# Optimization experiments

Measured on AMD Instinct MI355X. Metric: run time of the kernel, lower is better.

Reference implementation:

```python
import jax, jax.numpy as jnp
import numpy as np
from jax import lax

NEG = -10000.0


def setup_inputs() -> dict:
    key = jax.random.key(0)
    ks = jax.random.split(key, 16)
    T, V, E, H, NT = 2048, 50000, 512, 512, 48  # H = per-direction hidden (hidden_dim//2)
    start, end = NT - 2, NT - 1

    def rn(k, shape, scale=0.05):
        return jax.random.normal(k, shape, jnp.float32) * scale

    words = jax.random.randint(ks[0], (T,), 0, V)
    embed = rn(ks[1], (V, E), 0.1)
    Wih_f = rn(ks[2], (4 * H, E)); Whh_f = rn(ks[3], (4 * H, H))
    bih_f = rn(ks[4], (4 * H,));   bhh_f = rn(ks[5], (4 * H,))
    Wih_b = rn(ks[6], (4 * H, E)); Whh_b = rn(ks[7], (4 * H, H))
    bih_b = rn(ks[8], (4 * H,));   bhh_b = rn(ks[9], (4 * H,))
    W_out = rn(ks[10], (NT, 2 * H)); b_out = rn(ks[11], (NT,))
    transitions = jax.random.normal(ks[12], (NT, NT), jnp.float32)
    # match __init__: no transition into START, none out of END
    transitions = transitions.at[start, :].set(NEG).at[:, end].set(NEG)
    h0 = rn(ks[13], (2, H), 1.0)  # [fwd, bwd] initial hidden (torch.randn in init_hidden)
    c0 = rn(ks[14], (2, H), 1.0)
    return dict(words=words, embed=embed,
                Wih_f=Wih_f, Whh_f=Whh_f, bih_f=bih_f, bhh_f=bhh_f,
                Wih_b=Wih_b, Whh_b=Whh_b, bih_b=bih_b, bhh_b=bhh_b,
                W_out=W_out, b_out=b_out, transitions=transitions,
                h0=h0, c0=c0, start_tag=start, end_tag=end)


def _lstm_dir(x, h0, c0, Wih, Whh, bih, bhh, reverse):
    # x: [T, E]. Precompute input contribution for all steps (one big GEMM).
    xW = x @ Wih.T + (bih + bhh)  # [T, 4H]

    def step(carry, g_in):
        h, c = carry
        g = g_in + h @ Whh.T  # [4H]
        i, f, gg, o = jnp.split(g, 4)
        i = jax.nn.sigmoid(i); f = jax.nn.sigmoid(f)
        gg = jnp.tanh(gg);     o = jax.nn.sigmoid(o)
        c = f * c + i * gg
        h = o * jnp.tanh(c)
        return (h, c), h

    _, hs = lax.scan(step, (h0, c0), xW, reverse=reverse)
    return hs  # [T, H], aligned with input time order


def reference(words, embed, Wih_f, Whh_f, bih_f, bhh_f,
              Wih_b, Whh_b, bih_b, bhh_b,
              W_out, b_out, transitions, h0, c0, start_tag, end_tag):
    x = embed[words]  # [T, E]
    hf = _lstm_dir(x, h0[0], c0[0], Wih_f, Whh_f, bih_f, bhh_f, reverse=False)
    hb = _lstm_dir(x, h0[1], c0[1], Wih_b, Whh_b, bih_b, bhh_b, reverse=True)
    frames = jnp.concatenate([hf, hb], axis=-1) @ W_out.T + b_out  # [T, NT] emissions

    nt = transitions.shape[0]
    tT = transitions.T  # tT[from, to]
    alpha0 = jnp.full((nt,), NEG, frames.dtype).at[start_tag].set(0.0)

    def vstep(alpha, frame):
        # smat[i, j] = alpha[i] + frame[j] + transitions[j, i]
        smat = alpha[:, None] + frame[None, :] + tT
        return smat.max(axis=0), jnp.argmax(smat, axis=0)

    alpha, backtrace = lax.scan(vstep, alpha0, frames)  # backtrace: [T, NT]
    final = alpha + transitions[end_tag]
    best_last = jnp.argmax(final)
    score = final[best_last]

    def back(tag, bp):
        prev = bp[tag]
        return prev, prev

    _, path_head = lax.scan(back, best_last, backtrace[1:], reverse=True)  # [T-1]
    best_path = jnp.concatenate([path_head, best_last[None]])  # [T]
    return score, best_path
```

## Files before the change

### kernel.cpp

```cpp
#include <hip/hip_runtime.h>

#define TT 2048
#define HH 512
#define EE 512
#define NTAGS 48
#define G4 2048
#define NWG 16
#define CANARY 1.0e30f

typedef float f4 __attribute__((ext_vector_type(4)));

#define OFF_XW    0ULL
#define OFF_HCAT  (OFF_XW   + 2ULL*TT*G4*4ULL)
#define OFF_FRM   (OFF_HCAT + (unsigned long long)TT*1024ULL*4ULL)
#define OFF_HBUF  (OFF_FRM  + (unsigned long long)TT*NTAGS*4ULL)
#define OFF_BP    (OFF_HBUF + 2ULL*4ULL*HH*4ULL)

__device__ __forceinline__ float fsig(float x) {
    return __builtin_amdgcn_rcpf(1.f + __expf(-x));
}
__device__ __forceinline__ float ftanh(float x) {
    return 1.f - 2.f*__builtin_amdgcn_rcpf(__expf(2.f*x) + 1.f);
}

__global__ __launch_bounds__(256) void k_xw(
    const int* __restrict__ words, const float* __restrict__ embed,
    const float* __restrict__ WihF, const float* __restrict__ WihB,
    const float* __restrict__ bihF, const float* __restrict__ bhhF,
    const float* __restrict__ bihB, const float* __restrict__ bhhB,
    float* __restrict__ xw, float* __restrict__ hbuf)
{
    const int tid = threadIdx.x;
    const int bx = blockIdx.x, by = blockIdx.y, dir = blockIdx.z;

    if (bx == 0 && by == 0) {
        for (int j = tid; j < 4*HH; j += 256)
            hbuf[dir*4*HH + j] = CANARY;
    }

    const float* Wih = dir ? WihB : WihF;
    const float* bi  = dir ? bihB : bihF;
    const float* bh  = dir ? bhhB : bhhF;

    __shared__ float sa[32][64];
    __shared__ float sb[32][64];
    __shared__ int   wds[64];
    if (tid < 64) wds[tid] = words[by*64 + tid];
    const int tx = tid & 15, ty = tid >> 4;
    float acc[4][4] = {};
    __syncthreads();

    for (int k0 = 0; k0 < EE; k0 += 32) {
        #pragma unroll
        for (int u = 0; u < 2; u++) {
            int idx = tid*2 + u;
            int row = idx >> 3, kq = idx & 7;
            float4 av = *(const float4*)&embed[(size_t)wds[row]*EE + k0 + kq*4];
            float4 bv = *(const float4*)&Wih[(size_t)(bx*64 + row)*EE + k0 + kq*4];
            sa[kq*4+0][row] = av.x; sa[kq*4+1][row] = av.y;
            sa[kq*4+2][row] = av.z; sa[kq*4+3][row] = av.w;
            sb[kq*4+0][row] = bv.x; sb[kq*4+1][row] = bv.y;
            sb[kq*4+2][row] = bv.z; sb[kq*4+3][row] = bv.w;
        }
        __syncthreads();
        #pragma unroll
        for (int k = 0; k < 32; k++) {
            float4 a = *(const float4*)&sa[k][ty*4];
            float4 b = *(const float4*)&sb[k][tx*4];
            acc[0][0] += a.x*b.x; acc[0][1] += a.x*b.y; acc[0][2] += a.x*b.z; acc[0][3] += a.x*b.w;
            acc[1][0] += a.y*b.x; acc[1][1] += a.y*b.y; acc[1][2] += a.y*b.z; acc[1][3] += a.y*b.w;
            acc[2][0] += a.z*b.x; acc[2][1] += a.z*b.y; acc[2][2] += a.z*b.z; acc[2][3] += a.z*b.w;
            acc[3][0] += a.w*b.x; acc[3][1] += a.w*b.y; acc[3][2] += a.w*b.z; acc[3][3] += a.w*b.w;
        }
        __syncthreads();
    }

    float* outp = xw + (size_t)dir*TT*G4;
    const int rbase = bx*64 + tx*4;
    float4 bi4 = *(const float4*)&bi[rbase];
    float4 bh4 = *(const float4*)&bh[rbase];
    float4 bias = make_float4(bi4.x+bh4.x, bi4.y+bh4.y, bi4.z+bh4.z, bi4.w+bh4.w);
    #pragma unroll
    for (int i = 0; i < 4; i++) {
        int t = by*64 + ty*4 + i;
        float4 v = make_float4(acc[i][0]+bias.x, acc[i][1]+bias.y,
                               acc[i][2]+bias.z, acc[i][3]+bias.w);
        *(float4*)&outp[(size_t)t*G4 + rbase] = v;
    }
}

__global__ __launch_bounds__(512, 2) void k_lstm(
    const float* __restrict__ WhhF, const float* __restrict__ WhhB,
    const float* __restrict__ h0, const float* __restrict__ c0,
    const float* __restrict__ xw,
    float* __restrict__ hbuf, float* __restrict__ hcat)
{
    const int bid = blockIdx.x;
    const int dir = bid >> 4;
    const int w   = bid & 15;
    const float* Whh = dir ? WhhB : WhhF;
    const float* xwD = xw + (size_t)dir*TT*G4;
    float* hb = hbuf + dir*4*HH;

    const int tid  = threadIdx.x;
    const int v    = tid >> 6;
    const int l    = tid & 63;
    const int hi   = l >> 4;
    const int k16  = l & 15;
    const int loc  = v*4 + hi;
    const int hidx = w*32 + loc;

    f4 wreg[4][8];
    {
        #pragma unroll
        for (int g = 0; g < 4; g++) {
            const f4* wr = (const f4*)&Whh[(size_t)(g*HH + hidx)*HH + k16*32];
            #pragma unroll
            for (int t = 0; t < 8; t++)
                asm volatile("global_load_dwordx4 %0, %1, off"
                             : "=v"(wreg[g][t]) : "v"(wr + t));
        }
        asm volatile("s_waitcnt vmcnt(0)" ::: "memory");
        __builtin_amdgcn_sched_barrier(0);
    }
    float c = 0.f;
    if (tid < 32) c = c0[dir*HH + w*32 + tid];

    __shared__ __align__(16) float hsh[2][16*36];
    __shared__ float gv[128];

    hsh[0][(tid>>5)*36 + (tid&31)] = h0[dir*HH + tid];
    __syncthreads();

    float xv = 0.f;
    if (k16 < 4) xv = xwD[(size_t)(dir ? TT-1 : 0)*G4 + k16*HH + hidx];

    for (int s = 0; s < TT; s++) {
        const float* hc = &hsh[s & 1][k16*36];
        f4 p = {0.f, 0.f, 0.f, 0.f};
        #pragma unroll
        for (int t = 0; t < 8; t++) {
            float4 hv = *(const float4*)&hc[4*t];
            p.x += wreg[0][t].x*hv.x; p.x += wreg[0][t].y*hv.y;
            p.x += wreg[0][t].z*hv.z; p.x += wreg[0][t].w*hv.w;
            p.y += wreg[1][t].x*hv.x; p.y += wreg[1][t].y*hv.y;
            p.y += wreg[1][t].z*hv.z; p.y += wreg[1][t].w*hv.w;
            p.z += wreg[2][t].x*hv.x; p.z += wreg[2][t].y*hv.y;
            p.z += wreg[2][t].z*hv.z; p.z += wreg[2][t].w*hv.w;
            p.w += wreg[3][t].x*hv.x; p.w += wreg[3][t].y*hv.y;
            p.w += wreg[3][t].z*hv.z; p.w += wreg[3][t].w*hv.w;
        }
        #pragma unroll
        for (int m = 1; m < 16; m <<= 1) {
            p.x += __shfl_xor(p.x, m);
            p.y += __shfl_xor(p.y, m);
            p.z += __shfl_xor(p.z, m);
            p.w += __shfl_xor(p.w, m);
        }
        if (k16 < 4) {
            float sv = (k16 == 0) ? p.x : (k16 == 1) ? p.y : (k16 == 2) ? p.z : p.w;
            gv[k16*32 + loc] = sv + xv;
        }
        __syncthreads();

        const int time = dir ? (TT-1-s) : s;
        if (tid < 32) {
            const int jc = w*32 + tid;
            float gi = gv[tid], gf = gv[32+tid], gg = gv[64+tid], go = gv[96+tid];
            float i_ = fsig(gi);
            float f_ = fsig(gf);
            float g_ = ftanh(gg);
            float o_ = fsig(go);
            c = f_*c + i_*g_;
            float hn = o_*ftanh(c);
            if (s+1 < TT) {
                asm volatile("s_waitcnt vmcnt(0)" ::: "memory");
                __hip_atomic_store(&hb[((s+1)&3)*HH + jc], hn,
                                   __ATOMIC_RELAXED, __HIP_MEMORY_SCOPE_AGENT);
                __hip_atomic_store(&hb[((s+3)&3)*HH + jc], CANARY,
                                   __ATOMIC_RELAXED, __HIP_MEMORY_SCOPE_AGENT);
            }
            hcat[(size_t)time*1024 + dir*HH + jc] = hn;
        }

        if (s+1 < TT) {
            float xv_next = 0.f;
            if (k16 < 4)
                xv_next = xwD[(size_t)(dir ? TT-2-s : s+1)*G4 + k16*HH + hidx];

            const float* addr = &hb[((s+1)&3)*HH + tid];
            float va, vb = CANARY; int guard = 0;
            asm volatile("global_load_dword %0, %1, off sc1"
                         : "=v"(va) : "v"(addr));
            for (;;) {
                asm volatile("global_load_dword %0, %1, off sc1"
                             : "=v"(vb) : "v"(addr));
                asm volatile("s_waitcnt vmcnt(1)" ::: "memory");
                __builtin_amdgcn_sched_barrier(0);
                if (va != CANARY) break;
                asm volatile("global_load_dword %0, %1, off sc1"
                             : "=v"(va) : "v"(addr));
                asm volatile("s_waitcnt vmcnt(1)" ::: "memory");
                __builtin_amdgcn_sched_barrier(0);
                if (vb != CANARY) break;
                if (++guard > (1<<14)) break;
            }
            asm volatile("s_waitcnt vmcnt(0)" ::: "memory");
            __builtin_amdgcn_sched_barrier(0);
            float hv = (va != CANARY) ? va : vb;
            hsh[(s+1)&1][(tid>>5)*36 + (tid&31)] = hv;
            xv = xv_next;
            __syncthreads();
        }
    }
}

__global__ __launch_bounds__(64) void k_frames(
    const float* __restrict__ hcat, const float* __restrict__ Wout,
    const float* __restrict__ bout, float* __restrict__ frames)
{
    const int t = blockIdx.x, tid = threadIdx.x;
    __shared__ float hrow[1024];
    const float4* src  = (const float4*)&hcat[(size_t)t*1024];
    float4* dst4 = (float4*)hrow;
    #pragma unroll
    for (int u = 0; u < 4; u++) dst4[u*64 + tid] = src[u*64 + tid];
    __syncthreads();
    if (tid < NTAGS) {
        float acc = bout[tid];
        const float4* wr = (const float4*)&Wout[(size_t)tid*1024];
        #pragma unroll 16
        for (int e = 0; e < 256; e++) {
            float4 wv = wr[e];
            float4 hv = dst4[e];
            acc += wv.x*hv.x + wv.y*hv.y + wv.z*hv.z + wv.w*hv.w;
        }
        frames[t*NTAGS + tid] = acc;
    }
}

#define CH 256
__global__ __launch_bounds__(256) void k_viterbi(
    const float* __restrict__ frames, const float* __restrict__ trans,
    const int* __restrict__ startp, const int* __restrict__ endp,
    unsigned char* __restrict__ bp, float* __restrict__ out)
{
    const int tid = threadIdx.x;
    const int grp = tid / NTAGS;
    const int j   = tid % NTAGS;
    __shared__ float alpha[2][NTAGS];
    __shared__ float red[4][NTAGS];
    __shared__ int   redarg[4][NTAGS];
    __shared__ float frbuf[2][NTAGS];
    __shared__ __align__(16) unsigned char bps[CH*NTAGS];
    __shared__ int s_tag;

    float tr[12];
    if (grp < 4) {
        #pragma unroll
        for (int u = 0; u < 12; u++) tr[u] = trans[j*NTAGS + grp*12 + u];
    }
    const int start_tag = *startp;
    if (tid < NTAGS) alpha[0][tid] = (tid == start_tag) ? 0.f : -10000.f;
    const bool is_pf = (tid >= 192 && tid < 192 + NTAGS);
    if (is_pf) frbuf[0][tid-192] = frames[tid-192];
    __syncthreads();

    for (int t = 0; t < TT; t++) {
        float fpre = 0.f;
        if (is_pf && t+1 < TT) fpre = frames[(t+1)*NTAGS + (tid-192)];
        if (grp < 4) {
            float best = -3.0e38f; int barg = 0;
            #pragma unroll
            for (int u = 0; u < 12; u++) {
                float sv = alpha[t&1][grp*12+u] + tr[u];
                if (sv > best) { best = sv; barg = grp*12+u; }
            }
            red[grp][j] = best; redarg[grp][j] = barg;
        }
        __syncthreads();
        if (tid < NTAGS) {
            float b = red[0][tid]; int a = redarg[0][tid];
            #pragma unroll
            for (int g2 = 1; g2 < 4; g2++) {
                float v = red[g2][tid];
                if (v > b) { b = v; a = redarg[g2][tid]; }
            }
            bp[t*NTAGS + tid] = (unsigned char)a;
            alpha[(t+1)&1][tid] = b + frbuf[t&1][tid];
        }
        __syncthreads();
        if (is_pf && t+1 < TT) frbuf[(t+1)&1][tid-192] = fpre;
    }

    if (tid == 0) {
        const int end_tag = *endp;
        float best = -3.0e38f; int bl = 0;
        for (int j2 = 0; j2 < NTAGS; j2++) {
            float v = alpha[0][j2] + trans[end_tag*NTAGS + j2];
            if (v > best) { best = v; bl = j2; }
        }
        out[0] = best;
        out[1 + TT - 1] = (float)bl;
        s_tag = bl;
    }
    __syncthreads();

    for (int base = TT - CH; base >= 0; base -= CH) {
        {
            const float4* srcr = (const float4*)&bp[(size_t)(base + tid)*NTAGS];
            float4* dstr = (float4*)&bps[tid*NTAGS];
            dstr[0] = srcr[0]; dstr[1] = srcr[1]; dstr[2] = srcr[2];
        }
        __syncthreads();
        if (tid == 0) {
            int tag = s_tag;
            const int thi = base + CH - 1;
            const int tlo = (base == 0) ? 1 : base;
            for (int t = thi; t >= tlo; t--) {
                tag = bps[(t - base)*NTAGS + tag];
                out[t] = (float)tag;
            }
            s_tag = tag;
        }
        __syncthreads();
    }
}

extern "C" void kernel_launch(void* const* d_in, const int* in_sizes, int n_in,
                              void* d_out, int out_size, void* d_ws, size_t ws_size,
                              hipStream_t stream)
{
    const int*   words = (const int*)  d_in[0];
    const float* embed = (const float*)d_in[1];
    const float* WihF  = (const float*)d_in[2];
    const float* WhhF  = (const float*)d_in[3];
    const float* bihF  = (const float*)d_in[4];
    const float* bhhF  = (const float*)d_in[5];
    const float* WihB  = (const float*)d_in[6];
    const float* WhhB  = (const float*)d_in[7];
    const float* bihB  = (const float*)d_in[8];
    const float* bhhB  = (const float*)d_in[9];
    const float* Wout  = (const float*)d_in[10];
    const float* bout  = (const float*)d_in[11];
    const float* trans = (const float*)d_in[12];
    const float* h0    = (const float*)d_in[13];
    const float* c0    = (const float*)d_in[14];
    const int*   startp= (const int*)  d_in[15];
    const int*   endp  = (const int*)  d_in[16];

    char* ws = (char*)d_ws;
    float* xw   = (float*)(ws + OFF_XW);
    float* hcat = (float*)(ws + OFF_HCAT);
    float* frm  = (float*)(ws + OFF_FRM);
    float* hbuf = (float*)(ws + OFF_HBUF);
    unsigned char* bp = (unsigned char*)(ws + OFF_BP);

    dim3 g1(32, 32, 2);
    k_xw<<<g1, 256, 0, stream>>>(words, embed, WihF, WihB, bihF, bhhF,
                                 bihB, bhhB, xw, hbuf);
    k_lstm<<<dim3(2*NWG), 512, 0, stream>>>(WhhF, WhhB, h0, c0, xw, hbuf, hcat);
    k_frames<<<dim3(TT), 64, 0, stream>>>(hcat, Wout, bout, frm);
    k_viterbi<<<dim3(1), 256, 0, stream>>>(frm, trans, startp, endp, bp, (float*)d_out);
}
```

Before: 4.992 ms.

## Poll full hidden slice directly into registers, drop LDS staging and barrier

Each thread now polls its own 32-element slice of the shared hidden-state buffer with eight vector loads and keeps it in registers. This removes the LDS staging array for h and the second per-step workgroup barrier. The gate scratch buffer is double-buffered so the single remaining barrier per step is enough. The trade-off is that every thread issues eight times more polling traffic to the global buffer, and a whole slice must be canary-free before the thread proceeds.

```diff
diff --git a/kernel.cpp b/kernel.cpp
--- a/kernel.cpp
+++ b/kernel.cpp
@@ -126,21 +126,27 @@
     float c = 0.f;
     if (tid < 32) c = c0[dir*HH + w*32 + tid];
 
-    __shared__ __align__(16) float hsh[2][16*36];
-    __shared__ float gv[128];
-
-    hsh[0][(tid>>5)*36 + (tid&31)] = h0[dir*HH + tid];
-    __syncthreads();
+    __shared__ float gv[2][128];
+
+    f4 hvv[8];
+    {
+        const f4* hp = (const f4*)&h0[dir*HH + k16*32];
+        #pragma unroll
+        for (int t = 0; t < 8; t++)
+            asm volatile("global_load_dwordx4 %0, %1, off"
+                         : "=v"(hvv[t]) : "v"(hp + t));
+        asm volatile("s_waitcnt vmcnt(0)" ::: "memory");
+        __builtin_amdgcn_sched_barrier(0);
+    }
 
     float xv = 0.f;
     if (k16 < 4) xv = xwD[(size_t)(dir ? TT-1 : 0)*G4 + k16*HH + hidx];
 
     for (int s = 0; s < TT; s++) {
-        const float* hc = &hsh[s & 1][k16*36];
         f4 p = {0.f, 0.f, 0.f, 0.f};
         #pragma unroll
         for (int t = 0; t < 8; t++) {
-            float4 hv = *(const float4*)&hc[4*t];
+            f4 hv = hvv[t];
             p.x += wreg[0][t].x*hv.x; p.x += wreg[0][t].y*hv.y;
             p.x += wreg[0][t].z*hv.z; p.x += wreg[0][t].w*hv.w;
             p.y += wreg[1][t].x*hv.x; p.y += wreg[1][t].y*hv.y;
@@ -159,14 +165,15 @@
         }
         if (k16 < 4) {
             float sv = (k16 == 0) ? p.x : (k16 == 1) ? p.y : (k16 == 2) ? p.z : p.w;
-            gv[k16*32 + loc] = sv + xv;
+            gv[s & 1][k16*32 + loc] = sv + xv;
         }
         __syncthreads();
 
         const int time = dir ? (TT-1-s) : s;
         if (tid < 32) {
             const int jc = w*32 + tid;
-            float gi = gv[tid], gf = gv[32+tid], gg = gv[64+tid], go = gv[96+tid];
+            float gi = gv[s&1][tid],    gf = gv[s&1][32+tid];
+            float gg = gv[s&1][64+tid], go = gv[s&1][96+tid];
             float i_ = fsig(gi);
             float f_ = fsig(gf);
             float g_ = ftanh(gg);
@@ -184,33 +191,26 @@
         }
 
         if (s+1 < TT) {
-            float xv_next = 0.f;
             if (k16 < 4)
-                xv_next = xwD[(size_t)(dir ? TT-2-s : s+1)*G4 + k16*HH + hidx];
-
-            const float* addr = &hb[((s+1)&3)*HH + tid];
-            float va, vb = CANARY; int guard = 0;
-            asm volatile("global_load_dword %0, %1, off sc1"
-                         : "=v"(va) : "v"(addr));
+                xv = xwD[(size_t)(dir ? TT-2-s : s+1)*G4 + k16*HH + hidx];
+
+            const f4* base = (const f4*)&hb[((s+1)&3)*HH + k16*32];
+            int guard = 0;
             for (;;) {
-                asm volatile("global_load_dword %0, %1, off sc1"
-                             : "=v"(vb) : "v"(addr));
-                asm volatile("s_waitcnt vmcnt(1)" ::: "memory");
+                #pragma unroll
+                for (int t = 0; t < 8; t++)
+                    asm volatile("global_load_dwordx4 %0, %1, off sc1"
+                                 : "=v"(hvv[t]) : "v"(base + t));
+                asm volatile("s_waitcnt vmcnt(0)" ::: "memory");
                 __builtin_amdgcn_sched_barrier(0);
-                if (va != CANARY) break;
-                asm volatile("global_load_dword %0, %1, off sc1"
-                             : "=v"(va) : "v"(addr));
-                asm volatile("s_waitcnt vmcnt(1)" ::: "memory");
-                __builtin_amdgcn_sched_barrier(0);
-                if (vb != CANARY) break;
-                if (++guard > (1<<14)) break;
-            }
-            asm volatile("s_waitcnt vmcnt(0)" ::: "memory");
-            __builtin_amdgcn_sched_barrier(0);
-            float hv = (va != CANARY) ? va : vb;
-            hsh[(s+1)&1][(tid>>5)*36 + (tid&31)] = hv;
-            xv = xv_next;
-            __syncthreads();
+                bool ok = true;
+                #pragma unroll
+                for (int t = 0; t < 8; t++)
+                    ok &= (hvv[t].x != CANARY) & (hvv[t].y != CANARY) &
+                          (hvv[t].z != CANARY) & (hvv[t].w != CANARY);
+                if (ok) break;
+                if (++guard > (1<<13)) break;
+            }
         }
     }
 }
```

Result: slower. 9.265 ms (+85.6%).
